# Performance work log

Hardware: AMD Instinct MI355X
Metric: run time of the kernel (lower is better)

## Reference

```python
import jax, jax.numpy as jnp
import numpy as np

B, T, F = 64, 1000, 512
H, KD = 8, 32
EPS = 1e-6


def setup_inputs() -> dict:
    key = jax.random.key(0)
    ks = jax.random.split(key, 12)
    s_in = 1.0 / np.sqrt(F)
    s_out = 1.0 / np.sqrt(H * KD)
    return {
        "x": jax.random.normal(ks[0], (B, T, F), jnp.float32),
        "q": jax.random.normal(ks[1], (F,), jnp.float32) * s_in,      # global_query (1,1,F) squeezed
        "Wq": jax.random.normal(ks[2], (F, H, KD), jnp.float32) * s_in,
        "bq": jnp.zeros((H, KD), jnp.float32),
        "Wk": jax.random.normal(ks[3], (F, H, KD), jnp.float32) * s_in,
        "bk": jnp.zeros((H, KD), jnp.float32),
        "Wv": jax.random.normal(ks[4], (F, H, KD), jnp.float32) * s_in,
        "bv": jnp.zeros((H, KD), jnp.float32),
        "Wo": jax.random.normal(ks[5], (H, KD, F), jnp.float32) * s_out,
        "bo": jnp.zeros((F,), jnp.float32),
        "Wd": jax.random.normal(ks[6], (F, F), jnp.float32) * s_in,    # Dense, use_bias=False
        "gamma": jnp.ones((F,), jnp.float32),
        "beta": jnp.zeros((F,), jnp.float32),
    }


def reference(x, q, Wq, bq, Wk, bk, Wv, bv, Wo, bo, Wd, gamma, beta):
    # Single learned query attends over full sequence (keras MultiHeadAttention semantics).
    qh = jnp.einsum('f,fhk->hk', q, Wq) + bq                   # (H, KD), shared across batch
    kh = jnp.einsum('btf,fhk->bthk', x, Wk) + bk               # (B, T, H, KD)
    vh = jnp.einsum('btf,fhk->bthk', x, Wv) + bv               # (B, T, H, KD)
    scale = 1.0 / jnp.sqrt(jnp.asarray(KD, x.dtype))
    scores = jnp.einsum('hk,bthk->bht', qh, kh) * scale        # (B, H, T)
    attn = jax.nn.softmax(scores, axis=-1)
    ctx = jnp.einsum('bht,bthk->bhk', attn, vh)                # (B, H, KD)
    pooled = jnp.einsum('bhk,hkf->bf', ctx, Wo) + bo           # (B, F) attention output proj
    out = pooled @ Wd                                          # Dense, no bias
    mu = jnp.mean(out, axis=-1, keepdims=True)
    var = jnp.mean(jnp.square(out - mu), axis=-1, keepdims=True)
    return (out - mu) * jax.lax.rsqrt(var + EPS) * gamma + beta
```

## Files before the change

### kernel.cpp

```cpp
#include <hip/hip_runtime.h>
#include <cstddef>

#define B_ 64
#define T_ 1000
#define F_ 512
#define H_ 8
#define KD_ 32
#define HK_ 256

__global__ __launch_bounds__(64) void k_qh(const float* __restrict__ q,
                                           const float* __restrict__ Wq,
                                           const float* __restrict__ bq,
                                           float* __restrict__ qh) {
    int hk = blockIdx.x;
    int lane = threadIdx.x;
    float s = 0.f;
    for (int f = lane; f < F_; f += 64) s += q[f] * Wq[(size_t)f * HK_ + hk];
    #pragma unroll
    for (int off = 32; off; off >>= 1) s += __shfl_down(s, off);
    if (lane == 0) qh[hk] = s + bq[hk];
}

__global__ __launch_bounds__(256) void k_wk(const float* __restrict__ qh,
                                            const float* __restrict__ Wk,
                                            const float* __restrict__ bk,
                                            float* __restrict__ wk,
                                            float* __restrict__ ck) {
    int f = blockIdx.x;
    int tid = threadIdx.x;
    __shared__ float red[256];
    red[tid] = qh[tid] * Wk[(size_t)f * HK_ + tid];
    __syncthreads();
    #pragma unroll
    for (int off = 16; off; off >>= 1) {
        if ((tid & 31) < off) red[tid] += red[tid + off];
        __syncthreads();
    }
    if ((tid & 31) == 0) wk[f * H_ + (tid >> 5)] = red[tid];
    if (f == 0 && tid < H_) {
        float c = 0.f;
        for (int k = 0; k < KD_; k++) c += qh[tid * KD_ + k] * bk[tid * KD_ + k];
        ck[tid] = c;
    }
}

__global__ __launch_bounds__(256) void k_scores(const float* __restrict__ x,
                                                const float* __restrict__ wk,
                                                const float* __restrict__ ck,
                                                float* __restrict__ scores) {
    int gtid = blockIdx.x * blockDim.x + threadIdx.x;
    int wid = gtid >> 6;
    int lane = threadIdx.x & 63;
    int nw = (gridDim.x * blockDim.x) >> 6;
    int f0 = lane * 8;
    float wreg[8][8];
    #pragma unroll
    for (int i = 0; i < 8; i++)
        #pragma unroll
        for (int h = 0; h < H_; h++) wreg[i][h] = wk[(f0 + i) * H_ + h];
    float ckr[8];
    #pragma unroll
    for (int h = 0; h < H_; h++) ckr[h] = ck[h];
    const float scale = 0.17677669529663687f;

    for (int row = wid; row < B_ * T_; row += nw) {
        const float4* xr = (const float4*)(x + (size_t)row * F_ + f0);
        float4 a = xr[0], bb = xr[1];
        float xv[8] = {a.x, a.y, a.z, a.w, bb.x, bb.y, bb.z, bb.w};
        float acc[8];
        #pragma unroll
        for (int h = 0; h < H_; h++) acc[h] = 0.f;
        #pragma unroll
        for (int i = 0; i < 8; i++)
            #pragma unroll
            for (int h = 0; h < H_; h++) acc[h] += xv[i] * wreg[i][h];
        #pragma unroll
        for (int h = 0; h < H_; h++)
            #pragma unroll
            for (int off = 32; off; off >>= 1) acc[h] += __shfl_xor(acc[h], off);
        if (lane < H_) {
            float v = acc[0];
            #pragma unroll
            for (int h = 1; h < H_; h++) v = (lane == h) ? acc[h] : v;
            int b = row / T_, t = row - b * T_;
            scores[((size_t)b * H_ + lane) * T_ + t] = (v + ckr[lane]) * scale;
        }
    }
}

__global__ __launch_bounds__(256) void k_softmax(float* __restrict__ scores) {
    int row = blockIdx.x;
    int tid = threadIdx.x;
    float* s = scores + (size_t)row * T_;
    __shared__ float red[256];
    float m = -1e30f;
    for (int t = tid; t < T_; t += 256) m = fmaxf(m, s[t]);
    red[tid] = m; __syncthreads();
    #pragma unroll
    for (int off = 128; off; off >>= 1) {
        if (tid < off) red[tid] = fmaxf(red[tid], red[tid + off]);
        __syncthreads();
    }
    m = red[0]; __syncthreads();
    float sum = 0.f;
    for (int t = tid; t < T_; t += 256) { float e = __expf(s[t] - m); s[t] = e; sum += e; }
    red[tid] = sum; __syncthreads();
    #pragma unroll
    for (int off = 128; off; off >>= 1) {
        if (tid < off) red[tid] += red[tid + off];
        __syncthreads();
    }
    float inv = 1.0f / red[0];
    for (int t = tid; t < T_; t += 256) s[t] *= inv;
}

__global__ __launch_bounds__(256) void k_xp(const float* __restrict__ x,
                                            const float* __restrict__ attn,
                                            float* __restrict__ xp) {
    int bid = blockIdx.x;
    int tc = bid & 3;
    int fc = (bid >> 2) & 1;
    int b  = bid >> 3;
    int tid = threadIdx.x;
    int t0 = tc * 250, f0 = fc * 256;
    __shared__ float at[H_][256];
    for (int i = tid; i < H_ * 250; i += 256) {
        int h = i / 250, t = i - h * 250;
        at[h][t] = attn[((size_t)b * H_ + h) * T_ + t0 + t];
    }
    __syncthreads();
    float acc[H_] = {0.f,0.f,0.f,0.f,0.f,0.f,0.f,0.f};
    const float* xb = x + ((size_t)b * T_ + t0) * F_ + f0 + tid;
    for (int t = 0; t < 250; t++) {
        float xv = xb[(size_t)t * F_];
        #pragma unroll
        for (int h = 0; h < H_; h++) acc[h] += at[h][t] * xv;
    }
    #pragma unroll
    for (int h = 0; h < H_; h++)
        atomicAdd(&xp[((size_t)b * H_ + h) * F_ + f0 + tid], acc[h]);
}

__global__ __launch_bounds__(256) void k_final(const float* __restrict__ xp,
                                               const float* __restrict__ Wv,
                                               const float* __restrict__ bv,
                                               const float* __restrict__ Wo,
                                               const float* __restrict__ bo,
                                               const float* __restrict__ Wd,
                                               const float* __restrict__ gamma,
                                               const float* __restrict__ beta,
                                               float* __restrict__ out) {
    int b = blockIdx.x;
    int tid = threadIdx.x;
    __shared__ float xps[H_ * F_];
    __shared__ float ctx[HK_];
    __shared__ float pooled[F_];
    __shared__ float red[256];
    for (int i = tid; i < H_ * F_; i += 256) xps[i] = xp[(size_t)b * H_ * F_ + i];
    __syncthreads();
    {
        int h = tid >> 5;
        float s = 0.f;
        for (int f = 0; f < F_; f++) s += xps[h * F_ + f] * Wv[(size_t)f * HK_ + tid];
        ctx[tid] = s + bv[tid];
    }
    __syncthreads();
    #pragma unroll
    for (int j = 0; j < 2; j++) {
        int f = tid + j * 256;
        float s = 0.f;
        for (int hk = 0; hk < HK_; hk++) s += ctx[hk] * Wo[(size_t)hk * F_ + f];
        pooled[f] = s + bo[f];
    }
    __syncthreads();
    float o[2];
    #pragma unroll
    for (int j = 0; j < 2; j++) {
        int f = tid + j * 256;
        float s = 0.f;
        for (int g = 0; g < F_; g++) s += pooled[g] * Wd[(size_t)g * F_ + f];
        o[j] = s;
    }
    red[tid] = o[0] + o[1]; __syncthreads();
    #pragma unroll
    for (int off = 128; off; off >>= 1) { if (tid < off) red[tid] += red[tid + off]; __syncthreads(); }
    float mu = red[0] * (1.0f / F_); __syncthreads();
    float d0 = o[0] - mu, d1 = o[1] - mu;
    red[tid] = d0 * d0 + d1 * d1; __syncthreads();
    #pragma unroll
    for (int off = 128; off; off >>= 1) { if (tid < off) red[tid] += red[tid + off]; __syncthreads(); }
    float rstd = rsqrtf(red[0] * (1.0f / F_) + 1e-6f);
    #pragma unroll
    for (int j = 0; j < 2; j++) {
        int f = tid + j * 256;
        out[(size_t)b * F_ + f] = (o[j] - mu) * rstd * gamma[f] + beta[f];
    }
}

extern "C" void kernel_launch(void* const* d_in, const int* in_sizes, int n_in,
                              void* d_out, int out_size, void* d_ws, size_t ws_size,
                              hipStream_t stream) {
    const float* x     = (const float*)d_in[0];
    const float* q     = (const float*)d_in[1];
    const float* Wq    = (const float*)d_in[2];
    const float* bq    = (const float*)d_in[3];
    const float* Wk    = (const float*)d_in[4];
    const float* bk    = (const float*)d_in[5];
    const float* Wv    = (const float*)d_in[6];
    const float* bv    = (const float*)d_in[7];
    const float* Wo    = (const float*)d_in[8];
    const float* bo    = (const float*)d_in[9];
    const float* Wd    = (const float*)d_in[10];
    const float* gamma = (const float*)d_in[11];
    const float* beta  = (const float*)d_in[12];
    float* out = (float*)d_out;

    char* ws = (char*)d_ws;
    float* qh     = (float*)(ws + 0);
    float* wk     = (float*)(ws + 4096);
    float* ck     = (float*)(ws + 20480);
    float* scores = (float*)(ws + 24576);
    float* xp     = (float*)(ws + 2097152);

    k_qh<<<HK_, 64, 0, stream>>>(q, Wq, bq, qh);
    k_wk<<<F_, 256, 0, stream>>>(qh, Wk, bk, wk, ck);
    k_scores<<<1024, 256, 0, stream>>>(x, wk, ck, scores);
    k_softmax<<<B_ * H_, 256, 0, stream>>>(scores);
    hipMemsetAsync(xp, 0, (size_t)B_ * H_ * F_ * sizeof(float), stream);
    k_xp<<<B_ * 8, 256, 0, stream>>>(x, scores, xp);
    k_final<<<B_, 256, 0, stream>>>(xp, Wv, bv, Wo, bo, Wd, gamma, beta, out);
}
```

Before: 335.2 us.

## Replace atomic xp accumulation with partial buffers and widen tail kernel to 512 threads

The attention-weighted sum of x is now split over 8 time chunks, each covering the full F dimension with float2 loads. Every chunk writes its own partial buffer, which removes the memset and the atomicAdds. The tail kernel sums the 8 partials, runs at 512 threads per block with the Wv reduction split in halves, and computes the layernorm statistics with wave shuffles in a single pass. The cost is extra partial-buffer traffic (8x B*H*F floats), and the one-pass E[x^2]-mu^2 variance is less numerically robust.

```diff
diff --git a/kernel.cpp b/kernel.cpp
--- a/kernel.cpp
+++ b/kernel.cpp
@@ -116,85 +116,112 @@
 
 __global__ __launch_bounds__(256) void k_xp(const float* __restrict__ x,
                                             const float* __restrict__ attn,
-                                            float* __restrict__ xp) {
+                                            float* __restrict__ xp_part) {
     int bid = blockIdx.x;
-    int tc = bid & 3;
-    int fc = (bid >> 2) & 1;
+    int tc = bid & 7;
     int b  = bid >> 3;
     int tid = threadIdx.x;
-    int t0 = tc * 250, f0 = fc * 256;
-    __shared__ float at[H_][256];
-    for (int i = tid; i < H_ * 250; i += 256) {
-        int h = i / 250, t = i - h * 250;
-        at[h][t] = attn[((size_t)b * H_ + h) * T_ + t0 + t];
-    }
-    __syncthreads();
-    float acc[H_] = {0.f,0.f,0.f,0.f,0.f,0.f,0.f,0.f};
-    const float* xb = x + ((size_t)b * T_ + t0) * F_ + f0 + tid;
-    for (int t = 0; t < 250; t++) {
-        float xv = xb[(size_t)t * F_];
-        #pragma unroll
-        for (int h = 0; h < H_; h++) acc[h] += at[h][t] * xv;
-    }
+    int t0 = tc * 125;
+    __shared__ float at[H_][128];
+    for (int i = tid; i < H_ * 128; i += 256) {
+        int h = i >> 7, t = i & 127;
+        at[h][t] = (t < 125) ? attn[((size_t)b * H_ + h) * T_ + t0 + t] : 0.f;
+    }
+    __syncthreads();
+    float acc[H_][2];
+    #pragma unroll
+    for (int h = 0; h < H_; h++) { acc[h][0] = 0.f; acc[h][1] = 0.f; }
+    const float2* xb = (const float2*)(x + ((size_t)b * T_ + t0) * F_) + tid;
+    for (int t = 0; t < 125; t++) {
+        float2 xv = xb[(size_t)t * 256];
+        #pragma unroll
+        for (int h = 0; h < H_; h++) {
+            float a = at[h][t];
+            acc[h][0] += a * xv.x;
+            acc[h][1] += a * xv.y;
+        }
+    }
+    float2* dst = (float2*)(xp_part + ((size_t)(tc * B_ + b) * H_) * F_);
     #pragma unroll
     for (int h = 0; h < H_; h++)
-        atomicAdd(&xp[((size_t)b * H_ + h) * F_ + f0 + tid], acc[h]);
-}
-
-__global__ __launch_bounds__(256) void k_final(const float* __restrict__ xp,
-                                               const float* __restrict__ Wv,
-                                               const float* __restrict__ bv,
-                                               const float* __restrict__ Wo,
-                                               const float* __restrict__ bo,
-                                               const float* __restrict__ Wd,
-                                               const float* __restrict__ gamma,
-                                               const float* __restrict__ beta,
-                                               float* __restrict__ out) {
+        dst[h * (F_ / 2) + tid] = make_float2(acc[h][0], acc[h][1]);
+}
+
+__global__ __launch_bounds__(512) void k_tail(const float* __restrict__ xp_part,
+                                              const float* __restrict__ Wv,
+                                              const float* __restrict__ bv,
+                                              const float* __restrict__ Wo,
+                                              const float* __restrict__ bo,
+                                              const float* __restrict__ Wd,
+                                              const float* __restrict__ gamma,
+                                              const float* __restrict__ beta,
+                                              float* __restrict__ out) {
     int b = blockIdx.x;
     int tid = threadIdx.x;
-    __shared__ float xps[H_ * F_];
-    __shared__ float ctx[HK_];
-    __shared__ float pooled[F_];
-    __shared__ float red[256];
-    for (int i = tid; i < H_ * F_; i += 256) xps[i] = xp[(size_t)b * H_ * F_ + i];
-    __syncthreads();
+    __shared__ float xs[H_ * F_];
+    __shared__ float ctx_s[HK_];
+    __shared__ float pooled_s[F_];
+    __shared__ float red[512];
+    __shared__ float stat[2];
+
+    for (int i = tid; i < H_ * F_; i += 512) {
+        float s = 0.f;
+        #pragma unroll
+        for (int p = 0; p < 8; p++)
+            s += xp_part[(size_t)(p * B_ + b) * (H_ * F_) + i];
+        xs[i] = s;
+    }
+    __syncthreads();
+
     {
-        int h = tid >> 5;
+        int hk = tid & 255;
+        int half = tid >> 8;
+        int h = hk >> 5;
         float s = 0.f;
-        for (int f = 0; f < F_; f++) s += xps[h * F_ + f] * Wv[(size_t)f * HK_ + tid];
-        ctx[tid] = s + bv[tid];
-    }
-    __syncthreads();
-    #pragma unroll
-    for (int j = 0; j < 2; j++) {
-        int f = tid + j * 256;
+        int fb = half * 256;
+        for (int j = 0; j < 256; j++) {
+            int f = fb + j;
+            s += xs[h * F_ + f] * Wv[(size_t)f * HK_ + hk];
+        }
+        red[tid] = s;
+        __syncthreads();
+        if (tid < 256) ctx_s[tid] = red[tid] + red[tid + 256] + bv[tid];
+    }
+    __syncthreads();
+
+    {
         float s = 0.f;
-        for (int hk = 0; hk < HK_; hk++) s += ctx[hk] * Wo[(size_t)hk * F_ + f];
-        pooled[f] = s + bo[f];
-    }
-    __syncthreads();
-    float o[2];
-    #pragma unroll
-    for (int j = 0; j < 2; j++) {
-        int f = tid + j * 256;
-        float s = 0.f;
-        for (int g = 0; g < F_; g++) s += pooled[g] * Wd[(size_t)g * F_ + f];
-        o[j] = s;
-    }
-    red[tid] = o[0] + o[1]; __syncthreads();
-    #pragma unroll
-    for (int off = 128; off; off >>= 1) { if (tid < off) red[tid] += red[tid + off]; __syncthreads(); }
-    float mu = red[0] * (1.0f / F_); __syncthreads();
-    float d0 = o[0] - mu, d1 = o[1] - mu;
-    red[tid] = d0 * d0 + d1 * d1; __syncthreads();
-    #pragma unroll
-    for (int off = 128; off; off >>= 1) { if (tid < off) red[tid] += red[tid + off]; __syncthreads(); }
-    float rstd = rsqrtf(red[0] * (1.0f / F_) + 1e-6f);
-    #pragma unroll
-    for (int j = 0; j < 2; j++) {
-        int f = tid + j * 256;
-        out[(size_t)b * F_ + f] = (o[j] - mu) * rstd * gamma[f] + beta[f];
-    }
+        for (int hk = 0; hk < HK_; hk++) s += ctx_s[hk] * Wo[(size_t)hk * F_ + tid];
+        pooled_s[tid] = s + bo[tid];
+    }
+    __syncthreads();
+
+    float o = 0.f;
+    for (int g = 0; g < F_; g++) o += pooled_s[g] * Wd[(size_t)g * F_ + tid];
+
+    {
+        float v1 = o, v2 = o * o;
+        #pragma unroll
+        for (int off = 32; off; off >>= 1) {
+            v1 += __shfl_down(v1, off);
+            v2 += __shfl_down(v2, off);
+        }
+        int lane = tid & 63, wid = tid >> 6;
+        if (lane == 0) { red[wid] = v1; red[8 + wid] = v2; }
+        __syncthreads();
+        if (tid == 0) {
+            float s1 = 0.f, s2 = 0.f;
+            #pragma unroll
+            for (int w = 0; w < 8; w++) { s1 += red[w]; s2 += red[8 + w]; }
+            float mu = s1 * (1.0f / F_);
+            float var = s2 * (1.0f / F_) - mu * mu;
+            stat[0] = mu;
+            stat[1] = rsqrtf(var + 1e-6f);
+        }
+        __syncthreads();
+    }
+    float mu = stat[0], rstd = stat[1];
+    out[(size_t)b * F_ + tid] = (o - mu) * rstd * gamma[tid] + beta[tid];
 }
 
 extern "C" void kernel_launch(void* const* d_in, const int* in_sizes, int n_in,
@@ -216,17 +243,16 @@
     float* out = (float*)d_out;
 
     char* ws = (char*)d_ws;
-    float* qh     = (float*)(ws + 0);
-    float* wk     = (float*)(ws + 4096);
-    float* ck     = (float*)(ws + 20480);
-    float* scores = (float*)(ws + 24576);
-    float* xp     = (float*)(ws + 2097152);
+    float* qh      = (float*)(ws + 0);
+    float* wk      = (float*)(ws + 4096);
+    float* ck      = (float*)(ws + 20480);
+    float* scores  = (float*)(ws + 24576);
+    float* xp_part = (float*)(ws + 2097152);
 
     k_qh<<<HK_, 64, 0, stream>>>(q, Wq, bq, qh);
     k_wk<<<F_, 256, 0, stream>>>(qh, Wk, bk, wk, ck);
     k_scores<<<1024, 256, 0, stream>>>(x, wk, ck, scores);
     k_softmax<<<B_ * H_, 256, 0, stream>>>(scores);
-    hipMemsetAsync(xp, 0, (size_t)B_ * H_ * F_ * sizeof(float), stream);
-    k_xp<<<B_ * 8, 256, 0, stream>>>(x, scores, xp);
-    k_final<<<B_, 256, 0, stream>>>(xp, Wv, bv, Wo, bo, Wd, gamma, beta, out);
-}
+    k_xp<<<B_ * 8, 256, 0, stream>>>(x, scores, xp_part);
+    k_tail<<<B_, 512, 0, stream>>>(xp_part, Wv, bv, Wo, bo, Wd, gamma, beta, out);
+}
```

Result: faster. 301.6 us (-10.0%).
